# Kernel tuning notes

Measured on AMD Instinct MI355X. Metric: run time of the kernel, lower is better.

The kernel has to match this reference:

```python
import jax, jax.numpy as jnp
import numpy as np

# Attention(d_model=1024, d_head=64, h=16, fastmax=True) -> fastmax_custom path with
# mask=True, normalize=True, temperature=1, a0=1, a1=1, lim=1, p=1, zero RPE.
B, N, D_MODEL, H, D_HEAD = 1, 2048, 1024, 16, 64
A0, A1, LIM = 1.0, 1.0, 1.0


def setup_inputs() -> dict:
    key = jax.random.key(0)
    ks = jax.random.split(key, 6)
    s = 1.0 / np.sqrt(D_MODEL).astype(np.float32)
    return {
        "X": jax.random.normal(ks[0], (B, N, D_MODEL), jnp.float32),
        "Wq": jax.random.normal(ks[1], (H * D_HEAD, D_MODEL), jnp.float32) * s,
        "Wk": jax.random.normal(ks[2], (H * D_HEAD, D_MODEL), jnp.float32) * s,
        "Wv": jax.random.normal(ks[3], (H * D_HEAD, D_MODEL), jnp.float32) * s,
        "Wo": jax.random.normal(ks[4], (D_MODEL, H * D_HEAD), jnp.float32) * s,
        "bo": jnp.zeros((D_MODEL,), jnp.float32),
    }


def _fastmax_causal_p1(q, k, v):
    # q,k,v: [b,h,n,d]. fastmax normalize: scale q,k so the max per-token L2 norm
    # (over the sequence, per batch-head) equals LIM; temperature forced to 1.
    qn = jnp.max(jnp.linalg.norm(q, axis=-1), axis=-1)[..., None, None]  # [b,h,1,1]
    kn = jnp.max(jnp.linalg.norm(k, axis=-1), axis=-1)[..., None, None]
    q = LIM * q / qn
    k = LIM * k / kn
    n = q.shape[2]
    # first-order (p=1) polynomial kernel attention, causal via prefix sums:
    #   score(i,j) = a0 + a1 * <q_i, k_j>,  j <= i
    kv = jnp.cumsum(k[..., :, None] * v[..., None, :], axis=2)  # [b,h,n,d,d]
    num = A0 * jnp.cumsum(v, axis=2) + A1 * jnp.einsum('bhnd,bhnde->bhne', q, kv)
    ksum = jnp.cumsum(k, axis=2)  # [b,h,n,d]
    den = A0 * jnp.arange(1, n + 1, dtype=q.dtype) + A1 * jnp.einsum('bhnd,bhnd->bhn', q, ksum)
    return num / den[..., None]


def reference(X, Wq, Wk, Wv, Wo, bo):
    b, n, _ = X.shape

    def heads(W):
        # [b,n,d_model] @ [d_model,h*d] -> [b,h,n,d]
        return (X @ W.T).reshape(b, n, H, D_HEAD).transpose(0, 2, 1, 3)

    q, k, v = heads(Wq), heads(Wk), heads(Wv)
    vh = _fastmax_causal_p1(q, k, v)                       # [b,h,n,d]
    vh = vh.transpose(0, 2, 1, 3).reshape(b, n, H * D_HEAD)
    return vh @ Wo.T + bo                                  # eval mode: dropout is identity
```

## Files before the change

### kernel.cpp

```cpp
#include <hip/hip_runtime.h>

#define N_SEQ 2048
#define NH 16
#define DH 64
#define CHUNK 64
#define NCHUNK 32

typedef float f32x4 __attribute__((ext_vector_type(4)));
typedef __bf16 bf16x8 __attribute__((ext_vector_type(8)));
typedef unsigned short u16x4 __attribute__((ext_vector_type(4)));
typedef unsigned short u16x8 __attribute__((ext_vector_type(8)));

static __device__ inline unsigned short f2b(float x) {
    unsigned int u = __builtin_bit_cast(unsigned int, x);
    unsigned int r = (u + 0x7fffu + ((u >> 16) & 1u)) >> 16;
    return (unsigned short)r;
}
static __device__ inline float b2f(unsigned short b) {
    return __builtin_bit_cast(float, (unsigned int)b << 16);
}
static __device__ inline int sw(int row, int col) {
    return row * 64 + (col ^ ((row & 7) << 3));
}

__global__ __launch_bounds__(256) void cast_all(
    const float* __restrict__ X, const float* __restrict__ Wq, const float* __restrict__ Wk,
    const float* __restrict__ Wv, const float* __restrict__ Wo,
    unsigned short* __restrict__ Xb, unsigned short* __restrict__ Wb,
    unsigned short* __restrict__ Wob, float* __restrict__ nrm) {
    if (blockIdx.x == 0 && threadIdx.x < 32) nrm[threadIdx.x] = 0.f;
    int i = blockIdx.x * 256 + threadIdx.x;
    const float* src; unsigned short* dst; int off;
    if (i < 524288)       { src = X;  dst = Xb;               off = i; }
    else if (i < 786432)  { src = Wq; dst = Wb;               off = i - 524288; }
    else if (i < 1048576) { src = Wk; dst = Wb + (1u << 20);  off = i - 786432; }
    else if (i < 1310720) { src = Wv; dst = Wb + (2u << 20);  off = i - 1048576; }
    else                  { src = Wo; dst = Wob;              off = i - 1310720; }
    float4 v = reinterpret_cast<const float4*>(src)[off];
    u16x4 o;
    o[0] = f2b(v.x); o[1] = f2b(v.y); o[2] = f2b(v.z); o[3] = f2b(v.w);
    reinterpret_cast<u16x4*>(dst)[off] = o;
}

static __device__ inline void gload_lds16(const unsigned short* g, unsigned short* l) {
    __builtin_amdgcn_global_load_lds(
        (const __attribute__((address_space(1))) unsigned int*)g,
        (__attribute__((address_space(3))) unsigned int*)l, 16, 0, 0);
}

template<int MODE, int BM, int BN, int BK>
__global__ __launch_bounds__(256, 3) void gemm_bf16(
    const unsigned short* __restrict__ A,
    const unsigned short* __restrict__ B,
    float* __restrict__ outf,
    unsigned short* __restrict__ outb,
    const float* __restrict__ bias,
    float* __restrict__ nrm,
    int M, int N, int K)
{
    __shared__ __align__(16) unsigned short As[BM][BK];
    __shared__ __align__(16) unsigned short Bs[BN][BK];
    __shared__ float pnorm[2][BM];

    constexpr int SLOTS = BK / 8;
    constexpr int RPL   = 64 / SLOTS;

    const int L = blockIdx.y * gridDim.x + blockIdx.x;
    const int cpx = (gridDim.x * gridDim.y) >> 3;
    const int tile = (L & 7) * cpx + (L >> 3);
    const int bn = tile / gridDim.y;
    const int bm = tile % gridDim.y;

    const int t = threadIdx.x;
    const int wave = t >> 6, lane = t & 63;
    const int wm = wave >> 1, wn = wave & 1;
    const int r16 = lane & 15, ks = lane >> 4;
    constexpr int MFRAG = BM / 32;
    constexpr int NFRAG = BN / 32;

    f32x4 acc[MFRAG][NFRAG] = {};

    const unsigned short* gA = A + (size_t)bm * BM * K;
    const unsigned short* gB = B + (size_t)bn * BN * K;
    const int lrow  = lane / SLOTS;
    const int lslot = lane % SLOTS;
    const int rsw = (r16 & 7);

    for (int k0 = 0; k0 < K; k0 += BK) {
        __syncthreads();
        #pragma unroll
        for (int g2 = 0; g2 < BM * SLOTS / 256; ++g2) {
            int r0 = wave * (BM / 4) + g2 * RPL;
            int srccol = ((lslot ^ ((r0 + lrow) & 7)) << 3);
            gload_lds16(&gA[(size_t)(r0 + lrow) * K + k0 + srccol], &As[r0][0]);
        }
        #pragma unroll
        for (int g2 = 0; g2 < BN * SLOTS / 256; ++g2) {
            int r0 = wave * (BN / 4) + g2 * RPL;
            int srccol = ((lslot ^ ((r0 + lrow) & 7)) << 3);
            gload_lds16(&gB[(size_t)(r0 + lrow) * K + k0 + srccol], &Bs[r0][0]);
        }
        __syncthreads();

        #pragma unroll
        for (int kk = 0; kk < BK / 32; ++kk) {
            const int sl = ((((kk << 2) + ks) ^ rsw) << 3);
            bf16x8 af[MFRAG], bfr[NFRAG];
            #pragma unroll
            for (int m = 0; m < MFRAG; ++m)
                af[m] = *reinterpret_cast<const bf16x8*>(&As[wm * (BM / 2) + m * 16 + r16][sl]);
            #pragma unroll
            for (int n = 0; n < NFRAG; ++n)
                bfr[n] = *reinterpret_cast<const bf16x8*>(&Bs[wn * (BN / 2) + n * 16 + r16][sl]);
            #pragma unroll
            for (int m = 0; m < MFRAG; ++m)
                #pragma unroll
                for (int n = 0; n < NFRAG; ++n)
                    acc[m][n] = __builtin_amdgcn_mfma_f32_16x16x32_bf16(af[m], bfr[n], acc[m][n], 0, 0, 0);
        }
    }

    #pragma unroll
    for (int m = 0; m < MFRAG; ++m) {
        int row0 = bm * BM + wm * (BM / 2) + m * 16 + ks * 4;
        #pragma unroll
        for (int n = 0; n < NFRAG; ++n) {
            int col = bn * BN + wn * (BN / 2) + n * 16 + r16;
            if (MODE == 0) {
                int wch = col >> 10, h = (col >> 6) & 15, d = col & 63;
                unsigned short* dst = outb + (size_t)wch * (NH * (size_t)N_SEQ * DH)
                                          + (size_t)h * N_SEQ * DH + d;
                #pragma unroll
                for (int j = 0; j < 4; ++j)
                    dst[(size_t)(row0 + j) * DH] = f2b(acc[m][n][j]);
            } else {
                float bv = bias[col];
                #pragma unroll
                for (int j = 0; j < 4; ++j)
                    outf[(size_t)(row0 + j) * N + col] = acc[m][n][j] + bv;
            }
        }
    }

    if constexpr (MODE == 0) {
        const int wch = bn >> 4;
        if (wch < 2) {
            const int h = bn & 15;
            #pragma unroll
            for (int m = 0; m < MFRAG; ++m)
                #pragma unroll
                for (int j = 0; j < 4; ++j) {
                    float rs = 0.f;
                    #pragma unroll
                    for (int n = 0; n < NFRAG; ++n) rs = fmaf(acc[m][n][j], acc[m][n][j], rs);
                    rs += __shfl_xor(rs, 1);
                    rs += __shfl_xor(rs, 2);
                    rs += __shfl_xor(rs, 4);
                    rs += __shfl_xor(rs, 8);
                    if (r16 == 0)
                        pnorm[wn][wm * (BM / 2) + m * 16 + ks * 4 + j] = rs;
                }
            __syncthreads();
            if (t < BM) {
                float s = pnorm[0][t] + pnorm[1][t];
                #pragma unroll
                for (int o = 1; o < 64; o <<= 1) s = fmaxf(s, __shfl_xor(s, o));
                if ((t & 63) == 0)
                    atomicMax(reinterpret_cast<unsigned int*>(&nrm[wch * 16 + h]),
                              __builtin_bit_cast(unsigned int, s));
            }
        }
    }
}

__global__ __launch_bounds__(256) void chunk_sums(const unsigned short* __restrict__ Kb,
                                                  const unsigned short* __restrict__ Vb,
                                                  unsigned short* __restrict__ Ssum,
                                                  float* __restrict__ zsum,
                                                  float* __restrict__ vssum) {
    const int h = blockIdx.x >> 5, c = blockIdx.x & 31;
    __shared__ __align__(16) unsigned short Kt[4096];
    __shared__ __align__(16) unsigned short Vt[4096];
    const size_t off = ((size_t)h * N_SEQ + c * CHUNK) * DH;
    const int t = threadIdx.x, lane = t & 63;

    {
        const int d = t & 63, j0 = (t >> 6) * 16;
        unsigned short rk[16], rv[16];
        #pragma unroll
        for (int i = 0; i < 16; ++i) {
            rk[i] = Kb[off + (size_t)(j0 + i) * DH + d];
            rv[i] = Vb[off + (size_t)(j0 + i) * DH + d];
        }
        u16x8 a, b;
        #pragma unroll
        for (int i = 0; i < 8; ++i) { a[i] = rk[i]; b[i] = rk[8 + i]; }
        *reinterpret_cast<u16x8*>(&Kt[sw(d, j0)]) = a;
        *reinterpret_cast<u16x8*>(&Kt[sw(d, j0 + 8)]) = b;
        #pragma unroll
        for (int i = 0; i < 8; ++i) { a[i] = rv[i]; b[i] = rv[8 + i]; }
        *reinterpret_cast<u16x8*>(&Vt[sw(d, j0)]) = a;
        *reinterpret_cast<u16x8*>(&Vt[sw(d, j0 + 8)]) = b;
    }
    __syncthreads();

    const int w = t >> 6, cl = lane & 15, g = lane >> 4;
    bf16x8 ak0 = *reinterpret_cast<const bf16x8*>(&Kt[sw(w * 16 + cl, g * 8)]);
    bf16x8 ak1 = *reinterpret_cast<const bf16x8*>(&Kt[sw(w * 16 + cl, 32 + g * 8)]);
    f32x4 acc[4] = {};
    #pragma unroll
    for (int et = 0; et < 4; ++et) {
        bf16x8 b0 = *reinterpret_cast<const bf16x8*>(&Vt[sw(et * 16 + cl, g * 8)]);
        bf16x8 b1 = *reinterpret_cast<const bf16x8*>(&Vt[sw(et * 16 + cl, 32 + g * 8)]);
        acc[et] = __builtin_amdgcn_mfma_f32_16x16x32_bf16(ak0, b0, acc[et], 0, 0, 0);
        acc[et] = __builtin_amdgcn_mfma_f32_16x16x32_bf16(ak1, b1, acc[et], 0, 0, 0);
    }
    unsigned short* So = Ssum + (size_t)blockIdx.x * (DH * DH);
    #pragma unroll
    for (int et = 0; et < 4; ++et)
        #pragma unroll
        for (int j = 0; j < 4; ++j)
            So[(size_t)(w * 16 + g * 4 + j) * DH + et * 16 + cl] = f2b(acc[et][j]);

    if (t < 64) {
        float z = 0.f;
        #pragma unroll
        for (int i = 0; i < 8; ++i) {
            u16x8 v = *reinterpret_cast<const u16x8*>(&Kt[sw(t, i * 8)]);
            #pragma unroll
            for (int k = 0; k < 8; ++k) z += b2f(v[k]);
        }
        zsum[(size_t)blockIdx.x * DH + t] = z;
    } else if (t < 128) {
        int e = t - 64;
        float z = 0.f;
        #pragma unroll
        for (int i = 0; i < 8; ++i) {
            u16x8 v = *reinterpret_cast<const u16x8*>(&Vt[sw(e, i * 8)]);
            #pragma unroll
            for (int k = 0; k < 8; ++k) z += b2f(v[k]);
        }
        vssum[(size_t)blockIdx.x * DH + e] = z;
    }
}

__global__ __launch_bounds__(256) void chunk_scan(unsigned short* __restrict__ Ssum,
                                                  float* __restrict__ zsum,
                                                  float* __restrict__ vssum) {
    const int b = blockIdx.x;
    if (b < 256) {
        const int h = b >> 4;
        const int e = (b & 15) * 256 + threadIdx.x;
        size_t base = (size_t)h * NCHUNK * (DH * DH) + e;
        float v[NCHUNK];
        #pragma unroll
        for (int c = 0; c < NCHUNK; ++c) v[c] = b2f(Ssum[base + (size_t)c * (DH * DH)]);
        float run = 0.f;
        #pragma unroll
        for (int c = 0; c < NCHUNK; ++c) { float tmp = v[c]; v[c] = run; run += tmp; }
        #pragma unroll
        for (int c = 0; c < NCHUNK; ++c) Ssum[base + (size_t)c * (DH * DH)] = f2b(v[c]);
    } else {
        const int g = (b - 256) * 256 + threadIdx.x;
        const int which = g >> 10, h = (g >> 6) & 15, e = g & 63;
        float* arr = which ? vssum : zsum;
        size_t base = (size_t)h * NCHUNK * DH + e;
        float v[NCHUNK];
        #pragma unroll
        for (int c = 0; c < NCHUNK; ++c) v[c] = arr[base + (size_t)c * DH];
        float run = 0.f;
        #pragma unroll
        for (int c = 0; c < NCHUNK; ++c) { float tmp = v[c]; v[c] = run; run += tmp; }
        #pragma unroll
        for (int c = 0; c < NCHUNK; ++c) arr[base + (size_t)c * DH] = v[c];
    }
}

__global__ __launch_bounds__(256) void intra_attn(
    const unsigned short* __restrict__ Qb, const unsigned short* __restrict__ Kb,
    const unsigned short* __restrict__ Vb,
    const unsigned short* __restrict__ Ssum, const float* __restrict__ zsum,
    const float* __restrict__ vssum, const float* __restrict__ nrm,
    unsigned short* __restrict__ vhb) {
    const int h = blockIdx.x >> 5, c = blockIdx.x & 31;
    __shared__ __align__(16) unsigned short Ql[4096];
    __shared__ __align__(16) unsigned short Kl[4096];
    __shared__ __align__(16) unsigned short Vt[4096];
    __shared__ __align__(16) unsigned short Sp[4096];
    __shared__ __align__(16) unsigned short Pl[4096];
    __shared__ float zp[DH], vsp[DH];

    const int t = threadIdx.x, lane = t & 63, w = t >> 6;
    const float alpha = 1.f / sqrtf(nrm[h] * nrm[16 + h]);
    const size_t off = ((size_t)h * N_SEQ + c * CHUNK) * DH;

    #pragma unroll
    for (int p = 0; p < 2; ++p) {
        int lin = t + p * 256;
        int row = lin >> 3, col = (lin & 7) * 8;
        u16x8 q = *reinterpret_cast<const u16x8*>(Qb + off + (size_t)row * DH + col);
        u16x8 k = *reinterpret_cast<const u16x8*>(Kb + off + (size_t)row * DH + col);
        *reinterpret_cast<u16x8*>(&Ql[sw(row, col)]) = q;
        *reinterpret_cast<u16x8*>(&Kl[sw(row, col)]) = k;
    }
    {
        const int e = t & 63, j0 = (t >> 6) * 16;
        unsigned short rv[16];
        #pragma unroll
        for (int i = 0; i < 16; ++i) rv[i] = Vb[off + (size_t)(j0 + i) * DH + e];
        u16x8 a, b;
        #pragma unroll
        for (int i = 0; i < 8; ++i) { a[i] = rv[i]; b[i] = rv[8 + i]; }
        *reinterpret_cast<u16x8*>(&Vt[sw(e, j0)]) = a;
        *reinterpret_cast<u16x8*>(&Vt[sw(e, j0 + 8)]) = b;
    }
    {
        const unsigned short* Sg = Ssum + (size_t)blockIdx.x * (DH * DH);
        const int e = t & 63, d0 = (t >> 6) * 16;
        u16x8 a, b;
        #pragma unroll
        for (int i = 0; i < 8; ++i) a[i] = f2b(alpha * b2f(Sg[(size_t)(d0 + i) * DH + e]));
        #pragma unroll
        for (int i = 0; i < 8; ++i) b[i] = f2b(alpha * b2f(Sg[(size_t)(d0 + 8 + i) * DH + e]));
        *reinterpret_cast<u16x8*>(&Sp[sw(e, d0)]) = a;
        *reinterpret_cast<u16x8*>(&Sp[sw(e, d0 + 8)]) = b;
    }
    if (t < 64) zp[t] = alpha * zsum[(size_t)blockIdx.x * DH + t];
    else if (t < 128) vsp[t - 64] = vssum[(size_t)blockIdx.x * DH + (t - 64)];
    __syncthreads();

    const int cl = lane & 15, g = lane >> 4;
    const int qrow = (w << 4) + cl;

    bf16x8 aq0 = *reinterpret_cast<const bf16x8*>(&Ql[sw(qrow, g * 8)]);
    bf16x8 aq1 = *reinterpret_cast<const bf16x8*>(&Ql[sw(qrow, 32 + g * 8)]);

    f32x4 acc[4] = {};
    #pragma unroll
    for (int et = 0; et < 4; ++et) {
        bf16x8 b0 = *reinterpret_cast<const bf16x8*>(&Sp[sw(et * 16 + cl, g * 8)]);
        bf16x8 b1 = *reinterpret_cast<const bf16x8*>(&Sp[sw(et * 16 + cl, 32 + g * 8)]);
        acc[et] = __builtin_amdgcn_mfma_f32_16x16x32_bf16(aq0, b0, acc[et], 0, 0, 0);
        acc[et] = __builtin_amdgcn_mfma_f32_16x16x32_bf16(aq1, b1, acc[et], 0, 0, 0);
    }
    f32x4 sacc[4] = {};
    #pragma unroll
    for (int kt = 0; kt < 4; ++kt) {
        bf16x8 b0 = *reinterpret_cast<const bf16x8*>(&Kl[sw(kt * 16 + cl, g * 8)]);
        bf16x8 b1 = *reinterpret_cast<const bf16x8*>(&Kl[sw(kt * 16 + cl, 32 + g * 8)]);
        sacc[kt] = __builtin_amdgcn_mfma_f32_16x16x32_bf16(aq0, b0, sacc[kt], 0, 0, 0);
        sacc[kt] = __builtin_amdgcn_mfma_f32_16x16x32_bf16(aq1, b1, sacc[kt], 0, 0, 0);
    }
    unsigned short* Pw = &Pl[w * 1024];
    float part[4] = {0.f, 0.f, 0.f, 0.f};
    #pragma unroll
    for (int kt = 0; kt < 4; ++kt) {
        int key = kt * 16 + cl;
        #pragma unroll
        for (int j = 0; j < 4; ++j) {
            int rr = g * 4 + j;
            int q = (w << 4) + rr;
            float s = (key <= q) ? fmaf(alpha, sacc[kt][j], 1.f) : 0.f;
            part[j] += s;
            Pw[rr * 64 + (key ^ ((rr & 7) << 3))] = f2b(s);
        }
    }
    #pragma unroll
    for (int j = 0; j < 4; ++j) {
        int q = (w << 4) + g * 4 + j;
        float qz = 0.f;
        #pragma unroll
        for (int m = 0; m < 4; ++m) {
            int d = cl + m * 16;
            qz = fmaf(b2f(Ql[sw(q, d)]), zp[d], qz);
        }
        part[j] += qz;
    }
    #pragma unroll
    for (int o = 1; o < 16; o <<= 1)
        #pragma unroll
        for (int j = 0; j < 4; ++j) part[j] += __shfl_xor(part[j], o);
    float invden[4];
    #pragma unroll
    for (int j = 0; j < 4; ++j) invden[j] = 1.f / ((float)(c * CHUNK) + part[j]);

    #pragma unroll
    for (int ks = 0; ks < 2; ++ks) {
        bf16x8 ap = *reinterpret_cast<const bf16x8*>(&Pw[cl * 64 + ((ks * 32 + g * 8) ^ ((cl & 7) << 3))]);
        #pragma unroll
        for (int et = 0; et < 4; ++et) {
            bf16x8 bv = *reinterpret_cast<const bf16x8*>(&Vt[sw(et * 16 + cl, ks * 32 + g * 8)]);
            acc[et] = __builtin_amdgcn_mfma_f32_16x16x32_bf16(ap, bv, acc[et], 0, 0, 0);
        }
    }
    #pragma unroll
    for (int et = 0; et < 4; ++et)
        #pragma unroll
        for (int j = 0; j < 4; ++j) {
            int q = (w << 4) + g * 4 + j;
            int e = et * 16 + cl;
            float o = (vsp[e] + acc[et][j]) * invden[j];
            vhb[(size_t)(c * CHUNK + q) * (NH * DH) + h * DH + e] = f2b(o);
        }
}

extern "C" void kernel_launch(void* const* d_in, const int* in_sizes, int n_in,
                              void* d_out, int out_size, void* d_ws, size_t ws_size,
                              hipStream_t stream) {
    const float* X  = (const float*)d_in[0];
    const float* Wq = (const float*)d_in[1];
    const float* Wk = (const float*)d_in[2];
    const float* Wv = (const float*)d_in[3];
    const float* Wo = (const float*)d_in[4];
    const float* bo = (const float*)d_in[5];
    float* out = (float*)d_out;

    char* w = (char*)d_ws;
    unsigned short* Xb   = (unsigned short*)(w);
    unsigned short* Wb   = (unsigned short*)(w + (4u  << 20));
    unsigned short* Wob  = (unsigned short*)(w + (10u << 20));
    unsigned short* Qb   = (unsigned short*)(w + (12u << 20));
    unsigned short* vhb  = (unsigned short*)(w + (24u << 20));
    float*          nrm  = (float*)(w + (28u << 20));
    unsigned short* Ssum = (unsigned short*)(w + (29u << 20));
    float*          zsum = (float*)(w + (34u << 20));
    float*          vssum= (float*)(w + (34u << 20) + (1u << 17));
    unsigned short* Kb = Qb + 2097152;
    unsigned short* Vb = Qb + 2u * 2097152;

    cast_all<<<6144, 256, 0, stream>>>(X, Wq, Wk, Wv, Wo, Xb, Wb, Wob, nrm);
    gemm_bf16<0, 128, 64, 128><<<dim3(48, 16), 256, 0, stream>>>(Xb, Wb, nullptr, Qb, nullptr, nrm, 2048, 3072, 1024);
    chunk_sums<<<512, 256, 0, stream>>>(Kb, Vb, Ssum, zsum, vssum);
    chunk_scan<<<264, 256, 0, stream>>>(Ssum, zsum, vssum);
    intra_attn<<<512, 256, 0, stream>>>(Qb, Kb, Vb, Ssum, zsum, vssum, nrm, vhb);
    gemm_bf16<1, 64, 64, 128><<<dim3(16, 32), 256, 0, stream>>>(vhb, Wob, out, nullptr, bo, nullptr, 2048, 1024, 1024);
}
```

Measured before the change: 61.75 us.

## Stage QKV GEMM epilogue through LDS, grid-stride cast, deeper K tile

The QKV GEMM epilogue now writes its bf16 tile into shared memory with a padded stride and then stores rows to global memory as 16-byte vectors, replacing scattered 2-byte stores. The cast kernel now processes four elements per thread with a grid-stride loop over a quarter of the previous grid. The output projection GEMM uses a K tile of 256 instead of 128. Together these aim to cut uncoalesced-store traffic and launch overhead. The larger K tile raises LDS use and may reduce occupancy, and the LDS-staged epilogue adds an extra barrier.

```diff
diff --git a/kernel.cpp b/kernel.cpp
--- a/kernel.cpp
+++ b/kernel.cpp
@@ -29,17 +29,20 @@
     unsigned short* __restrict__ Xb, unsigned short* __restrict__ Wb,
     unsigned short* __restrict__ Wob, float* __restrict__ nrm) {
     if (blockIdx.x == 0 && threadIdx.x < 32) nrm[threadIdx.x] = 0.f;
-    int i = blockIdx.x * 256 + threadIdx.x;
-    const float* src; unsigned short* dst; int off;
-    if (i < 524288)       { src = X;  dst = Xb;               off = i; }
-    else if (i < 786432)  { src = Wq; dst = Wb;               off = i - 524288; }
-    else if (i < 1048576) { src = Wk; dst = Wb + (1u << 20);  off = i - 786432; }
-    else if (i < 1310720) { src = Wv; dst = Wb + (2u << 20);  off = i - 1048576; }
-    else                  { src = Wo; dst = Wob;              off = i - 1310720; }
-    float4 v = reinterpret_cast<const float4*>(src)[off];
-    u16x4 o;
-    o[0] = f2b(v.x); o[1] = f2b(v.y); o[2] = f2b(v.z); o[3] = f2b(v.w);
-    reinterpret_cast<u16x4*>(dst)[off] = o;
+    #pragma unroll
+    for (int it = 0; it < 4; ++it) {
+        int i = blockIdx.x * 256 + threadIdx.x + it * 393216;
+        const float* src; unsigned short* dst; int off;
+        if (i < 524288)       { src = X;  dst = Xb;               off = i; }
+        else if (i < 786432)  { src = Wq; dst = Wb;               off = i - 524288; }
+        else if (i < 1048576) { src = Wk; dst = Wb + (1u << 20);  off = i - 786432; }
+        else if (i < 1310720) { src = Wv; dst = Wb + (2u << 20);  off = i - 1048576; }
+        else                  { src = Wo; dst = Wob;              off = i - 1310720; }
+        float4 v = reinterpret_cast<const float4*>(src)[off];
+        u16x4 o;
+        o[0] = f2b(v.x); o[1] = f2b(v.y); o[2] = f2b(v.z); o[3] = f2b(v.w);
+        reinterpret_cast<u16x4*>(dst)[off] = o;
+    }
 }
 
 static __device__ inline void gload_lds16(const unsigned short* g, unsigned short* l) {
@@ -120,32 +123,23 @@
         }
     }
 
-    #pragma unroll
-    for (int m = 0; m < MFRAG; ++m) {
-        int row0 = bm * BM + wm * (BM / 2) + m * 16 + ks * 4;
-        #pragma unroll
-        for (int n = 0; n < NFRAG; ++n) {
-            int col = bn * BN + wn * (BN / 2) + n * 16 + r16;
-            if (MODE == 0) {
-                int wch = col >> 10, h = (col >> 6) & 15, d = col & 63;
-                unsigned short* dst = outb + (size_t)wch * (NH * (size_t)N_SEQ * DH)
-                                          + (size_t)h * N_SEQ * DH + d;
+    if constexpr (MODE == 0) {
+        __syncthreads();
+        unsigned short* Ct = &As[0][0];
+        #pragma unroll
+        for (int m = 0; m < MFRAG; ++m)
+            #pragma unroll
+            for (int n = 0; n < NFRAG; ++n) {
+                int col = wn * (BN / 2) + n * 16 + r16;
                 #pragma unroll
-                for (int j = 0; j < 4; ++j)
-                    dst[(size_t)(row0 + j) * DH] = f2b(acc[m][n][j]);
-            } else {
-                float bv = bias[col];
-                #pragma unroll
-                for (int j = 0; j < 4; ++j)
-                    outf[(size_t)(row0 + j) * N + col] = acc[m][n][j] + bv;
+                for (int j = 0; j < 4; ++j) {
+                    int row = wm * (BM / 2) + m * 16 + ks * 4 + j;
+                    Ct[row * 80 + col] = f2b(acc[m][n][j]);
+                }
             }
-        }
-    }
-
-    if constexpr (MODE == 0) {
         const int wch = bn >> 4;
+        const int h = bn & 15;
         if (wch < 2) {
-            const int h = bn & 15;
             #pragma unroll
             for (int m = 0; m < MFRAG; ++m)
                 #pragma unroll
@@ -160,14 +154,36 @@
                     if (r16 == 0)
                         pnorm[wn][wm * (BM / 2) + m * 16 + ks * 4 + j] = rs;
                 }
-            __syncthreads();
-            if (t < BM) {
-                float s = pnorm[0][t] + pnorm[1][t];
+        }
+        __syncthreads();
+        unsigned short* dstb = outb + (size_t)wch * (NH * (size_t)N_SEQ * DH)
+                                    + (size_t)h * N_SEQ * DH;
+        #pragma unroll
+        for (int pass = 0; pass < BM / 32; ++pass) {
+            int row = pass * 32 + (t >> 3);
+            int dcol = (t & 7) * 8;
+            u16x8 vv = *reinterpret_cast<const u16x8*>(&Ct[row * 80 + dcol]);
+            *reinterpret_cast<u16x8*>(&dstb[(size_t)(bm * BM + row) * DH + dcol]) = vv;
+        }
+        if (wch < 2 && t < BM) {
+            float s = pnorm[0][t] + pnorm[1][t];
+            #pragma unroll
+            for (int o = 1; o < 64; o <<= 1) s = fmaxf(s, __shfl_xor(s, o));
+            if ((t & 63) == 0)
+                atomicMax(reinterpret_cast<unsigned int*>(&nrm[wch * 16 + h]),
+                          __builtin_bit_cast(unsigned int, s));
+        }
+    } else {
+        #pragma unroll
+        for (int m = 0; m < MFRAG; ++m) {
+            int row0 = bm * BM + wm * (BM / 2) + m * 16 + ks * 4;
+            #pragma unroll
+            for (int n = 0; n < NFRAG; ++n) {
+                int col = bn * BN + wn * (BN / 2) + n * 16 + r16;
+                float bv = bias[col];
                 #pragma unroll
-                for (int o = 1; o < 64; o <<= 1) s = fmaxf(s, __shfl_xor(s, o));
-                if ((t & 63) == 0)
-                    atomicMax(reinterpret_cast<unsigned int*>(&nrm[wch * 16 + h]),
-                              __builtin_bit_cast(unsigned int, s));
+                for (int j = 0; j < 4; ++j)
+                    outf[(size_t)(row0 + j) * N + col] = acc[m][n][j] + bv;
             }
         }
     }
@@ -428,10 +444,10 @@
     unsigned short* Kb = Qb + 2097152;
     unsigned short* Vb = Qb + 2u * 2097152;
 
-    cast_all<<<6144, 256, 0, stream>>>(X, Wq, Wk, Wv, Wo, Xb, Wb, Wob, nrm);
+    cast_all<<<1536, 256, 0, stream>>>(X, Wq, Wk, Wv, Wo, Xb, Wb, Wob, nrm);
     gemm_bf16<0, 128, 64, 128><<<dim3(48, 16), 256, 0, stream>>>(Xb, Wb, nullptr, Qb, nullptr, nrm, 2048, 3072, 1024);
     chunk_sums<<<512, 256, 0, stream>>>(Kb, Vb, Ssum, zsum, vssum);
     chunk_scan<<<264, 256, 0, stream>>>(Ssum, zsum, vssum);
     intra_attn<<<512, 256, 0, stream>>>(Qb, Kb, Vb, Ssum, zsum, vssum, nrm, vhb);
-    gemm_bf16<1, 64, 64, 128><<<dim3(16, 32), 256, 0, stream>>>(vhb, Wob, out, nullptr, bo, nullptr, 2048, 1024, 1024);
-}
+    gemm_bf16<1, 64, 64, 256><<<dim3(16, 32), 256, 0, stream>>>(vhb, Wob, out, nullptr, bo, nullptr, 2048, 1024, 1024);
+}
```

Measured after the change: 60.63 us. About the same (-1.8%).
